# Optimization experiments

Measured on AMD Instinct MI355X. Metric: run time of the kernel, lower is better.

Reference implementation:

```python
import math
import jax, jax.numpy as jnp
import numpy as np

C = 32        # per-head dim
N_HEAD = 8
C_IN = 128

def setup_inputs() -> dict:
    key = jax.random.key(0)
    ks = jax.random.split(key, 10)
    B, S = 1, 256
    sc = 0.05  # keep logits in a sane range
    x    = jax.random.normal(ks[0], (B, S, S, C_IN), dtype=jnp.float32)
    bias = jax.random.normal(ks[1], (B, N_HEAD, S, S), dtype=jnp.float32)
    attention_mask = jax.random.randint(ks[2], (B, S, S), 0, 2).astype(bool)
    Wq = jax.random.normal(ks[3], (C_IN, C * N_HEAD), dtype=jnp.float32) * sc
    Wk = jax.random.normal(ks[4], (C_IN, C * N_HEAD), dtype=jnp.float32) * sc
    Wv = jax.random.normal(ks[5], (C_IN, C * N_HEAD), dtype=jnp.float32) * sc
    Wo = jax.random.normal(ks[6], (C * N_HEAD, C_IN), dtype=jnp.float32) * sc
    bo = jnp.zeros((C_IN,), dtype=jnp.float32)
    Wg = jax.random.normal(ks[7], (C_IN, C * N_HEAD), dtype=jnp.float32) * sc
    bg = jnp.zeros((C * N_HEAD,), dtype=jnp.float32)
    return {"x": x, "bias": bias, "attention_mask": attention_mask,
            "Wq": Wq, "Wk": Wk, "Wv": Wv, "Wo": Wo, "bo": bo, "Wg": Wg, "bg": bg}

def reference(x, bias, attention_mask, Wq, Wk, Wv, Wo, bo, Wg, bg):
    # x: [B, S, L, c_in]; attn_dim=2 is already the second-to-last dim,
    # so the torch movedim(attn_dim, -2) is the identity here.
    B, S, L, _ = x.shape
    q = x @ Wq  # [B, S, L, H*c]
    k = x @ Wk
    v = x @ Wv
    # split heads: [B, S, L, H, c] -> [B, S, H, L, c]
    def split_heads(t):
        return t.reshape(B, S, L, N_HEAD, C).transpose(0, 1, 3, 2, 4)
    q, k, v = split_heads(q), split_heads(k), split_heads(v)
    q = q / math.sqrt(C)
    # attention logits: [B, S, H, q, k]
    a = jnp.einsum('bshqc,bshkc->bshqk', q, k)
    # bias [B, H, q, k] -> broadcast over the axial batch dim S
    a = a + bias[:, None, :, :, :]
    # mask [B, S, k] -> [B, S, 1, 1, k]; masked positions get -inf
    m = attention_mask[:, :, None, None, :]
    a = jnp.where(m, a, -jnp.inf)
    a = jax.nn.softmax(a, axis=-1)
    o = jnp.einsum('bshqk,bshkc->bshqc', a, v)
    # merge heads: [B, S, H, L, c] -> [B, S, L, H*c]
    o = o.transpose(0, 1, 3, 2, 4).reshape(B, S, L, N_HEAD * C)
    # sigmoid gate
    g = jax.nn.sigmoid(x @ Wg + bg)
    o = g * o
    return o @ Wo + bo
```

## Files before the change

### kernel.cpp

```cpp
#include <hip/hip_runtime.h>
#include <hip/hip_bf16.h>
#include <cstdint>

#define CIN 128
#define NH 8
#define CH 32
#define LDQ16 1024

typedef short bf16x8 __attribute__((ext_vector_type(8)));
typedef short bf16x4 __attribute__((ext_vector_type(4)));
typedef float f32x4 __attribute__((ext_vector_type(4)));

__device__ __forceinline__ short f2bf(float f) {
  union { float f; unsigned u; } v; v.f = f;
  unsigned r = (v.u + 0x7FFFu + ((v.u >> 16) & 1u)) >> 16;
  return (short)r;
}
__device__ __forceinline__ float bf2f(short s) {
  union { unsigned u; float f; } v; v.u = ((unsigned)(unsigned short)s) << 16;
  return v.f;
}
__device__ __forceinline__ unsigned pk2bf(float a, float b) {
  union { __hip_bfloat162 h; unsigned u; } cv;
  cv.h = __float22bfloat162_rn(make_float2(a, b));
  return cv.u;
}

__global__ __launch_bounds__(256) void prep(
    const float* __restrict__ x,
    const float* __restrict__ Wq, const float* __restrict__ Wk,
    const float* __restrict__ Wv, const float* __restrict__ Wg,
    const float* __restrict__ Wo,
    const uint4* __restrict__ mask,
    short* __restrict__ xb, short* __restrict__ WT, short* __restrict__ WoT,
    unsigned int* __restrict__ flag)
{
  __shared__ int viol;
  const int b = blockIdx.x;
  if (b < 4096) {
    int base = (b * 256 + threadIdx.x) * 8;
    float4 a = *(const float4*)(x + base);
    float4 c = *(const float4*)(x + base + 4);
    bf16x8 r;
    r[0] = f2bf(a.x); r[1] = f2bf(a.y); r[2] = f2bf(a.z); r[3] = f2bf(a.w);
    r[4] = f2bf(c.x); r[5] = f2bf(c.y); r[6] = f2bf(c.z); r[7] = f2bf(c.w);
    *(bf16x8*)(xb + base) = r;
  } else if (b < 4160) {
    const float qscale = 0.17677669529663689f;
    int bb = b - 4096;
#pragma unroll
    for (int e = 0; e < 10; ++e) {
      int o = bb * 2560 + e * 256 + threadIdx.x;
      if (o < 131072) {
        int n = o >> 7, k = o & 127;
        int seg = n >> 8, nn = n & 255;
        const float* W = (seg == 0) ? Wq : (seg == 1) ? Wk : (seg == 2) ? Wv : Wg;
        float v = W[k * 256 + nn];
        if (seg == 0) v *= qscale;
        WT[o] = f2bf(v);
      } else {
        int o2 = o - 131072;
        int n = o2 >> 8, k = o2 & 255;
        WoT[o2] = f2bf(Wo[k * 128 + n]);
      }
    }
  } else {
    if (threadIdx.x == 0) viol = 0;
    __syncthreads();
    int v = 0;
#pragma unroll
    for (int j = 0; j < 16; ++j) {
      uint4 w = mask[j * 256 + threadIdx.x];
      v |= (w.x > 1u) | (w.y > 1u) | (w.z > 1u) | (w.w > 1u);
    }
    if (v) atomicOr(&viol, 1);
    __syncthreads();
    if (threadIdx.x == 0) *flag = viol ? 0u : 1u;
  }
}

__global__ __launch_bounds__(256) void proj_qkvg(
    const short* __restrict__ xb, const short* __restrict__ WT,
    const float* __restrict__ bg, short* __restrict__ qkvg)
{
  __shared__ short Al[64 * 136];
  __shared__ short Bl[128 * 136];
  const int tid = threadIdx.x;
  const int lane = tid & 63, w = tid >> 6;
  const int g = lane >> 4, c16 = lane & 15;
  const int wr = w & 1, wc = w >> 1;
  const int n0 = blockIdx.x * 128;
  const int row0 = blockIdx.y * 64;

  {
    const short* src = xb + (size_t)row0 * 128;
#pragma unroll
    for (int ch = 0; ch < 4; ++ch) {
      int c = ch * 256 + tid;
      int r = c >> 4, kc = c & 15;
      *(bf16x8*)&Al[r * 136 + kc * 8] = *(const bf16x8*)(src + r * 128 + kc * 8);
    }
    const short* wsrc = WT + (size_t)n0 * 128;
#pragma unroll
    for (int ch = 0; ch < 8; ++ch) {
      int c = ch * 256 + tid;
      int r = c >> 4, kc = c & 15;
      *(bf16x8*)&Bl[r * 136 + kc * 8] = *(const bf16x8*)(wsrc + r * 128 + kc * 8);
    }
  }
  __syncthreads();

  f32x4 acc[2][4];
#pragma unroll
  for (int rt = 0; rt < 2; ++rt)
#pragma unroll
    for (int ct = 0; ct < 4; ++ct) acc[rt][ct] = (f32x4){0.f, 0.f, 0.f, 0.f};

#pragma unroll
  for (int kk = 0; kk < 4; ++kk) {
    bf16x8 af[2], bfr[4];
#pragma unroll
    for (int rt = 0; rt < 2; ++rt)
      af[rt] = *(const bf16x8*)&Al[(wr * 32 + rt * 16 + c16) * 136 + kk * 32 + g * 8];
#pragma unroll
    for (int ct = 0; ct < 4; ++ct)
      bfr[ct] = *(const bf16x8*)&Bl[(wc * 64 + ct * 16 + c16) * 136 + kk * 32 + g * 8];
#pragma unroll
    for (int rt = 0; rt < 2; ++rt)
#pragma unroll
      for (int ct = 0; ct < 4; ++ct)
        acc[rt][ct] = __builtin_amdgcn_mfma_f32_16x16x32_bf16(af[rt], bfr[ct], acc[rt][ct], 0, 0, 0);
  }

  const int seg3 = (n0 >= 768);
  float bgv[4];
  if (seg3) {
#pragma unroll
    for (int ct = 0; ct < 4; ++ct)
      bgv[ct] = bg[n0 - 768 + wc * 64 + ct * 16 + c16];
  }
#pragma unroll
  for (int rt = 0; rt < 2; ++rt)
#pragma unroll
    for (int ct = 0; ct < 4; ++ct) {
      int col = n0 + wc * 64 + ct * 16 + c16;
#pragma unroll
      for (int i = 0; i < 4; ++i) {
        int row = row0 + wr * 32 + rt * 16 + g * 4 + i;
        float v = acc[rt][ct][i];
        if (seg3) v = 1.f / (1.f + __expf(-(v + bgv[ct])));
        qkvg[(size_t)row * LDQ16 + col] = f2bf(v);
      }
    }
}

__global__ __launch_bounds__(256, 4) void attn(
    short* __restrict__ qkvg, const float* __restrict__ bias,
    const void* __restrict__ maskraw, const unsigned int* __restrict__ flagp)
{
  __shared__ __align__(16) short lds16[19216];
  const int tid = threadIdx.x;
  const int h = blockIdx.x;
  const int srow = blockIdx.y;
  const int lane = tid & 63, w = tid >> 6;
  const int g = lane >> 4, c16 = lane & 15;
  short* rowbase = qkvg + (size_t)srow * (256 * LDQ16);
  unsigned int* vTd = (unsigned int*)&lds16[10240];
  float* lL = (float*)&lds16[18688];

  const unsigned int fl = *flagp;
  int mv = fl ? ((const int*)maskraw)[srow * 256 + tid]
              : (int)((const unsigned char*)maskraw)[srow * 256 + tid];
  unsigned long long bb = __ballot(mv != 0);
  unsigned int* scratch = (unsigned int*)&lds16[19200];
  if (lane == 0) {
    scratch[w * 2 + 0] = (unsigned int)bb;
    scratch[w * 2 + 1] = (unsigned int)(bb >> 32);
  }

#pragma unroll
  for (int it = 0; it < 2; ++it) {
    int c = it * 256 + tid;
    int kp = c >> 2, cv = c & 3;
    const short* p0 = rowbase + (size_t)(2 * kp) * LDQ16 + 256 + h * CH + cv * 8;
    bf16x8 k0 = *(const bf16x8*)p0;
    bf16x8 k1 = *(const bf16x8*)(p0 + LDQ16);
    bf16x8 v0 = *(const bf16x8*)(p0 + 256);
    bf16x8 v1 = *(const bf16x8*)(p0 + LDQ16 + 256);
    *(bf16x8*)&lds16[(2 * kp) * 40 + cv * 8] = k0;
    *(bf16x8*)&lds16[(2 * kp + 1) * 40 + cv * 8] = k1;
#pragma unroll
    for (int j = 0; j < 8; ++j)
      vTd[(cv * 8 + j) * 132 + kp] =
          ((unsigned)(unsigned short)v0[j]) | (((unsigned)(unsigned short)v1[j]) << 16);
  }

  const int qb = w * 64;
  bf16x8 qf[4];
#pragma unroll
  for (int qt = 0; qt < 4; ++qt)
    qf[qt] = *(const bf16x8*)(rowbase + (size_t)(qb + qt * 16 + c16) * LDQ16 + h * CH + g * 8);

  __syncthreads();

  unsigned int mb[8];
#pragma unroll
  for (int j = 0; j < 8; ++j) mb[j] = scratch[j];

  const f32x4 zero4 = {0.f, 0.f, 0.f, 0.f};
  float l_[4] = {0.f, 0.f, 0.f, 0.f};
  f32x4 O[4][2];
#pragma unroll
  for (int qt = 0; qt < 4; ++qt) { O[qt][0] = zero4; O[qt][1] = zero4; }

  const float* bh = bias + (size_t)h * 65536;

  for (int ch = 0; ch < 8; ++ch) {
    float4 bb4[2][4];
#pragma unroll
    for (int kt = 0; kt < 2; ++kt)
#pragma unroll
      for (int qt = 0; qt < 4; ++qt)
        bb4[kt][qt] = *(const float4*)(bh + (size_t)(qb + qt * 16 + c16) * 256 +
                                       ch * 32 + kt * 16 + g * 4);

#pragma unroll
    for (int kt = 0; kt < 2; ++kt) {
      bf16x8 kf = *(const bf16x8*)&lds16[(ch * 32 + kt * 16 + c16) * 40 + g * 8];
      bf16x4 vlo, vhi;
      {
        union { unsigned u[2]; bf16x4 v; } t0, t1;
        const unsigned* plo = &vTd[(size_t)c16 * 132 + ch * 16 + kt * 8 + g * 2];
        const unsigned* phi = &vTd[(size_t)(16 + c16) * 132 + ch * 16 + kt * 8 + g * 2];
        t0.u[0] = plo[0]; t0.u[1] = plo[1];
        t1.u[0] = phi[0]; t1.u[1] = phi[1];
        vlo = t0.v; vhi = t1.v;
      }
      const unsigned nib = (mb[ch] >> (kt * 16 + g * 4)) & 0xFu;
      float em[4];
#pragma unroll
      for (int i = 0; i < 4; ++i) em[i] = ((nib >> i) & 1u) ? 1.f : 0.f;
#pragma unroll
      for (int qt = 0; qt < 4; ++qt) {
        f32x4 S = __builtin_amdgcn_mfma_f32_16x16x32_bf16(kf, qf[qt], zero4, 0, 0, 0);
        float p0 = em[0] * __expf(fminf(S[0] + bb4[kt][qt].x, 85.f));
        float p1 = em[1] * __expf(fminf(S[1] + bb4[kt][qt].y, 85.f));
        float p2 = em[2] * __expf(fminf(S[2] + bb4[kt][qt].z, 85.f));
        float p3 = em[3] * __expf(fminf(S[3] + bb4[kt][qt].w, 85.f));
        l_[qt] += (p0 + p1) + (p2 + p3);
        union { unsigned u[2]; bf16x4 v; } pu;
        pu.u[0] = pk2bf(p0, p1);
        pu.u[1] = pk2bf(p2, p3);
        O[qt][0] = __builtin_amdgcn_mfma_f32_16x16x16bf16_1k(pu.v, vlo, O[qt][0], 0, 0, 0);
        O[qt][1] = __builtin_amdgcn_mfma_f32_16x16x16bf16_1k(pu.v, vhi, O[qt][1], 0, 0, 0);
      }
    }
  }

#pragma unroll
  for (int qt = 0; qt < 4; ++qt) {
    float v = l_[qt];
    v += __shfl_xor(v, 16);
    v += __shfl_xor(v, 32);
    if (lane < 16) lL[w * 64 + qt * 16 + c16] = v;
  }

#pragma unroll
  for (int qt = 0; qt < 4; ++qt)
#pragma unroll
    for (int i = 0; i < 4; ++i) {
      float l = lL[w * 64 + qt * 16 + g * 4 + i];
      float inv = 1.f / l;
      short* orow = rowbase + (size_t)(qb + qt * 16 + g * 4 + i) * LDQ16;
#pragma unroll
      for (int half = 0; half < 2; ++half) {
        int c = half * 16 + c16;
        float gv = bf2f(orow[768 + h * CH + c]);
        orow[h * CH + c] = f2bf(O[qt][half][i] * inv * gv);
      }
    }
}

__global__ __launch_bounds__(256) void out_proj(
    const short* __restrict__ og, const short* __restrict__ WoT,
    const float* __restrict__ bo, float* __restrict__ out)
{
  __shared__ short Al[64 * 136];
  __shared__ short Bl[128 * 136];
  const int tid = threadIdx.x;
  const int lane = tid & 63, w = tid >> 6;
  const int g = lane >> 4, c16 = lane & 15;
  const int wr = w & 1, wc = w >> 1;
  const int row0 = blockIdx.x * 64;

  f32x4 acc[2][4];
#pragma unroll
  for (int rt = 0; rt < 2; ++rt)
#pragma unroll
    for (int ct = 0; ct < 4; ++ct) acc[rt][ct] = (f32x4){0.f, 0.f, 0.f, 0.f};

  for (int kk0 = 0; kk0 < 256; kk0 += 128) {
#pragma unroll
    for (int ch = 0; ch < 4; ++ch) {
      int c = ch * 256 + tid;
      int r = c >> 4, kc = c & 15;
      *(bf16x8*)&Al[r * 136 + kc * 8] =
          *(const bf16x8*)(og + (size_t)(row0 + r) * LDQ16 + kk0 + kc * 8);
    }
#pragma unroll
    for (int ch = 0; ch < 8; ++ch) {
      int c = ch * 256 + tid;
      int r = c >> 4, kc = c & 15;
      *(bf16x8*)&Bl[r * 136 + kc * 8] =
          *(const bf16x8*)(WoT + (size_t)r * 256 + kk0 + kc * 8);
    }
    __syncthreads();
#pragma unroll
    for (int kk = 0; kk < 4; ++kk) {
      bf16x8 af[2], bfr[4];
#pragma unroll
      for (int rt = 0; rt < 2; ++rt)
        af[rt] = *(const bf16x8*)&Al[(wr * 32 + rt * 16 + c16) * 136 + kk * 32 + g * 8];
#pragma unroll
      for (int ct = 0; ct < 4; ++ct)
        bfr[ct] = *(const bf16x8*)&Bl[(wc * 64 + ct * 16 + c16) * 136 + kk * 32 + g * 8];
#pragma unroll
      for (int rt = 0; rt < 2; ++rt)
#pragma unroll
        for (int ct = 0; ct < 4; ++ct)
          acc[rt][ct] = __builtin_amdgcn_mfma_f32_16x16x32_bf16(af[rt], bfr[ct], acc[rt][ct], 0, 0, 0);
    }
    __syncthreads();
  }

#pragma unroll
  for (int rt = 0; rt < 2; ++rt)
#pragma unroll
    for (int ct = 0; ct < 4; ++ct) {
      int col = wc * 64 + ct * 16 + c16;
      float bv = bo[col];
#pragma unroll
      for (int i = 0; i < 4; ++i) {
        int row = row0 + wr * 32 + rt * 16 + g * 4 + i;
        out[(size_t)row * CIN + col] = acc[rt][ct][i] + bv;
      }
    }
}

extern "C" void kernel_launch(void* const* d_in, const int* in_sizes, int n_in,
                              void* d_out, int out_size, void* d_ws, size_t ws_size,
                              hipStream_t stream) {
  const float* x    = (const float*)d_in[0];
  const float* bias = (const float*)d_in[1];
  const void*  mask = d_in[2];
  const float* Wq   = (const float*)d_in[3];
  const float* Wk   = (const float*)d_in[4];
  const float* Wv   = (const float*)d_in[5];
  const float* Wo   = (const float*)d_in[6];
  const float* bo   = (const float*)d_in[7];
  const float* Wg   = (const float*)d_in[8];
  const float* bg   = (const float*)d_in[9];
  float* out = (float*)d_out;

  unsigned int* flag = (unsigned int*)d_ws;
  short* WT   = (short*)((char*)d_ws + 256);
  short* WoT  = WT + 131072;
  short* xb   = WoT + 32768;
  short* qkvg = xb + (size_t)65536 * 128;

  prep<<<4161, 256, 0, stream>>>(x, Wq, Wk, Wv, Wg, Wo, (const uint4*)mask,
                                 xb, WT, WoT, flag);
  proj_qkvg<<<dim3(8, 1024), 256, 0, stream>>>(xb, WT, bg, qkvg);
  attn<<<dim3(NH, 256), 256, 0, stream>>>(qkvg, bias, mask, flag);
  out_proj<<<1024, 256, 0, stream>>>(qkvg, WoT, bo, out);
}
```

Baseline: 259.8 us.

## Read K directly from global, shrink LDS, use exp2 with pre-scaled Q and bias

The attention kernel stops staging K in LDS and loads K fragments straight from global memory (L2-cached), which cuts LDS use roughly in half and lets launch bounds request 8 blocks per CU instead of 4. The softmax exponential switches from expf to exp2. To keep results unchanged, log2(e) is folded into the Q weight scale and into a pre-scaled copy of the bias produced by extra blocks in the prep kernel. In exchange, K loads now sit on the global-memory path inside the inner loop, prep does an extra pass over the bias tensor, and the higher occupancy target may squeeze registers.

```diff
diff --git a/kernel.cpp b/kernel.cpp
--- a/kernel.cpp
+++ b/kernel.cpp
@@ -30,10 +30,10 @@
     const float* __restrict__ x,
     const float* __restrict__ Wq, const float* __restrict__ Wk,
     const float* __restrict__ Wv, const float* __restrict__ Wg,
-    const float* __restrict__ Wo,
+    const float* __restrict__ Wo, const float* __restrict__ bias,
     const uint4* __restrict__ mask,
     short* __restrict__ xb, short* __restrict__ WT, short* __restrict__ WoT,
-    unsigned int* __restrict__ flag)
+    float* __restrict__ biasX, unsigned int* __restrict__ flag)
 {
   __shared__ int viol;
   const int b = blockIdx.x;
@@ -46,7 +46,7 @@
     r[4] = f2bf(c.x); r[5] = f2bf(c.y); r[6] = f2bf(c.z); r[7] = f2bf(c.w);
     *(bf16x8*)(xb + base) = r;
   } else if (b < 4160) {
-    const float qscale = 0.17677669529663689f;
+    const float qscale = 0.25504430213978686f;
     int bb = b - 4096;
 #pragma unroll
     for (int e = 0; e < 10; ++e) {
@@ -64,6 +64,12 @@
         WoT[o2] = f2bf(Wo[k * 128 + n]);
       }
     }
+  } else if (b < 4672) {
+    const float LOG2E = 1.4426950408889634f;
+    int idx = ((b - 4160) * 256 + threadIdx.x) * 4;
+    float4 v = *(const float4*)(bias + idx);
+    v.x *= LOG2E; v.y *= LOG2E; v.z *= LOG2E; v.w *= LOG2E;
+    *(float4*)(biasX + idx) = v;
   } else {
     if (threadIdx.x == 0) viol = 0;
     __syncthreads();
@@ -154,25 +160,25 @@
     }
 }
 
-__global__ __launch_bounds__(256, 4) void attn(
+__global__ __launch_bounds__(256, 8) void attn(
     short* __restrict__ qkvg, const float* __restrict__ bias,
     const void* __restrict__ maskraw, const unsigned int* __restrict__ flagp)
 {
-  __shared__ __align__(16) short lds16[19216];
+  __shared__ __align__(16) short lds16[8976];
   const int tid = threadIdx.x;
   const int h = blockIdx.x;
   const int srow = blockIdx.y;
   const int lane = tid & 63, w = tid >> 6;
   const int g = lane >> 4, c16 = lane & 15;
   short* rowbase = qkvg + (size_t)srow * (256 * LDQ16);
-  unsigned int* vTd = (unsigned int*)&lds16[10240];
-  float* lL = (float*)&lds16[18688];
+  unsigned int* vTd = (unsigned int*)&lds16[0];
+  float* lL = (float*)&lds16[8448];
+  unsigned int* scratch = (unsigned int*)&lds16[8960];
 
   const unsigned int fl = *flagp;
   int mv = fl ? ((const int*)maskraw)[srow * 256 + tid]
               : (int)((const unsigned char*)maskraw)[srow * 256 + tid];
   unsigned long long bb = __ballot(mv != 0);
-  unsigned int* scratch = (unsigned int*)&lds16[19200];
   if (lane == 0) {
     scratch[w * 2 + 0] = (unsigned int)bb;
     scratch[w * 2 + 1] = (unsigned int)(bb >> 32);
@@ -182,13 +188,9 @@
   for (int it = 0; it < 2; ++it) {
     int c = it * 256 + tid;
     int kp = c >> 2, cv = c & 3;
-    const short* p0 = rowbase + (size_t)(2 * kp) * LDQ16 + 256 + h * CH + cv * 8;
-    bf16x8 k0 = *(const bf16x8*)p0;
-    bf16x8 k1 = *(const bf16x8*)(p0 + LDQ16);
-    bf16x8 v0 = *(const bf16x8*)(p0 + 256);
-    bf16x8 v1 = *(const bf16x8*)(p0 + LDQ16 + 256);
-    *(bf16x8*)&lds16[(2 * kp) * 40 + cv * 8] = k0;
-    *(bf16x8*)&lds16[(2 * kp + 1) * 40 + cv * 8] = k1;
+    const short* p0 = rowbase + (size_t)(2 * kp) * LDQ16 + 512 + h * CH + cv * 8;
+    bf16x8 v0 = *(const bf16x8*)p0;
+    bf16x8 v1 = *(const bf16x8*)(p0 + LDQ16);
 #pragma unroll
     for (int j = 0; j < 8; ++j)
       vTd[(cv * 8 + j) * 132 + kp] =
@@ -201,6 +203,8 @@
   for (int qt = 0; qt < 4; ++qt)
     qf[qt] = *(const bf16x8*)(rowbase + (size_t)(qb + qt * 16 + c16) * LDQ16 + h * CH + g * 8);
 
+  const short* kb = rowbase + (size_t)c16 * LDQ16 + 256 + h * CH + g * 8;
+
   __syncthreads();
 
   unsigned int mb[8];
@@ -226,7 +230,7 @@
 
 #pragma unroll
     for (int kt = 0; kt < 2; ++kt) {
-      bf16x8 kf = *(const bf16x8*)&lds16[(ch * 32 + kt * 16 + c16) * 40 + g * 8];
+      bf16x8 kf = *(const bf16x8*)(kb + (size_t)((ch * 32 + kt * 16) * LDQ16));
       bf16x4 vlo, vhi;
       {
         union { unsigned u[2]; bf16x4 v; } t0, t1;
@@ -243,10 +247,10 @@
 #pragma unroll
       for (int qt = 0; qt < 4; ++qt) {
         f32x4 S = __builtin_amdgcn_mfma_f32_16x16x32_bf16(kf, qf[qt], zero4, 0, 0, 0);
-        float p0 = em[0] * __expf(fminf(S[0] + bb4[kt][qt].x, 85.f));
-        float p1 = em[1] * __expf(fminf(S[1] + bb4[kt][qt].y, 85.f));
-        float p2 = em[2] * __expf(fminf(S[2] + bb4[kt][qt].z, 85.f));
-        float p3 = em[3] * __expf(fminf(S[3] + bb4[kt][qt].w, 85.f));
+        float p0 = em[0] * __builtin_exp2f(fminf(S[0] + bb4[kt][qt].x, 122.f));
+        float p1 = em[1] * __builtin_exp2f(fminf(S[1] + bb4[kt][qt].y, 122.f));
+        float p2 = em[2] * __builtin_exp2f(fminf(S[2] + bb4[kt][qt].z, 122.f));
+        float p3 = em[3] * __builtin_exp2f(fminf(S[3] + bb4[kt][qt].w, 122.f));
         l_[qt] += (p0 + p1) + (p2 + p3);
         union { unsigned u[2]; bf16x4 v; } pu;
         pu.u[0] = pk2bf(p0, p1);
@@ -367,10 +371,11 @@
   short* WoT  = WT + 131072;
   short* xb   = WoT + 32768;
   short* qkvg = xb + (size_t)65536 * 128;
-
-  prep<<<4161, 256, 0, stream>>>(x, Wq, Wk, Wv, Wg, Wo, (const uint4*)mask,
-                                 xb, WT, WoT, flag);
+  float* biasX = (float*)(qkvg + (size_t)65536 * 1024);
+
+  prep<<<4673, 256, 0, stream>>>(x, Wq, Wk, Wv, Wg, Wo, bias, (const uint4*)mask,
+                                 xb, WT, WoT, biasX, flag);
   proj_qkvg<<<dim3(8, 1024), 256, 0, stream>>>(xb, WT, bg, qkvg);
-  attn<<<dim3(NH, 256), 256, 0, stream>>>(qkvg, bias, mask, flag);
+  attn<<<dim3(NH, 256), 256, 0, stream>>>(qkvg, biasX, mask, flag);
   out_proj<<<1024, 256, 0, stream>>>(qkvg, WoT, bo, out);
 }
```

After: 759.0 us. +192.2%, slower.

## Fuse x conversion, QKVG projection and attention into one per-row kernel

Applied to the files above, without the earlier changes.

Drops the separate x-to-bf16 pass and the QKVG projection kernel. A new fused kernel, one block of 512 threads per axial row, loads x once into LDS and computes Q, K, V and gate for each head on the fly. It then runs attention from LDS and writes only the gated output (256 columns instead of 1024). This removes the large qkvg intermediate round trip through HBM. In exchange only 256 blocks run, each with heavy LDS use, and every block re-reads the weights from global memory with heads processed serially, so occupancy and parallelism drop.

```diff
diff --git a/kernel.cpp b/kernel.cpp
--- a/kernel.cpp
+++ b/kernel.cpp
@@ -5,7 +5,6 @@
 #define CIN 128
 #define NH 8
 #define CH 32
-#define LDQ16 1024
 
 typedef short bf16x8 __attribute__((ext_vector_type(8)));
 typedef short bf16x4 __attribute__((ext_vector_type(4)));
@@ -27,30 +26,20 @@
 }
 
 __global__ __launch_bounds__(256) void prep(
-    const float* __restrict__ x,
     const float* __restrict__ Wq, const float* __restrict__ Wk,
     const float* __restrict__ Wv, const float* __restrict__ Wg,
     const float* __restrict__ Wo,
     const uint4* __restrict__ mask,
-    short* __restrict__ xb, short* __restrict__ WT, short* __restrict__ WoT,
+    short* __restrict__ WT, short* __restrict__ WoT,
     unsigned int* __restrict__ flag)
 {
   __shared__ int viol;
   const int b = blockIdx.x;
-  if (b < 4096) {
-    int base = (b * 256 + threadIdx.x) * 8;
-    float4 a = *(const float4*)(x + base);
-    float4 c = *(const float4*)(x + base + 4);
-    bf16x8 r;
-    r[0] = f2bf(a.x); r[1] = f2bf(a.y); r[2] = f2bf(a.z); r[3] = f2bf(a.w);
-    r[4] = f2bf(c.x); r[5] = f2bf(c.y); r[6] = f2bf(c.z); r[7] = f2bf(c.w);
-    *(bf16x8*)(xb + base) = r;
-  } else if (b < 4160) {
+  if (b < 64) {
     const float qscale = 0.17677669529663689f;
-    int bb = b - 4096;
 #pragma unroll
     for (int e = 0; e < 10; ++e) {
-      int o = bb * 2560 + e * 256 + threadIdx.x;
+      int o = b * 2560 + e * 256 + threadIdx.x;
       if (o < 131072) {
         int n = o >> 7, k = o & 127;
         int seg = n >> 8, nn = n & 255;
@@ -79,206 +68,266 @@
   }
 }
 
-__global__ __launch_bounds__(256) void proj_qkvg(
-    const short* __restrict__ xb, const short* __restrict__ WT,
-    const float* __restrict__ bg, short* __restrict__ qkvg)
+__global__ __launch_bounds__(512) void fused_attn(
+    const float* __restrict__ x, const short* __restrict__ WT,
+    const float* __restrict__ bias, const float* __restrict__ bg,
+    const void* __restrict__ maskraw, const unsigned int* __restrict__ flagp,
+    short* __restrict__ og)
 {
-  __shared__ short Al[64 * 136];
-  __shared__ short Bl[128 * 136];
+  __shared__ __align__(16) short xl[256 * 136];
+  __shared__ __align__(16) short kL[256 * 40];
+  __shared__ __align__(16) short vL[32 * 264];
+  __shared__ __align__(16) short qL[256 * 40];
+  __shared__ __align__(16) short gL[256 * 40];
+  __shared__ float lL[256];
+  __shared__ unsigned int scratch[8];
+
   const int tid = threadIdx.x;
+  const int srow = blockIdx.x;
   const int lane = tid & 63, w = tid >> 6;
   const int g = lane >> 4, c16 = lane & 15;
-  const int wr = w & 1, wc = w >> 1;
-  const int n0 = blockIdx.x * 128;
-  const int row0 = blockIdx.y * 64;
+  const int myrow = w * 32;
+
+  const unsigned int fl = *flagp;
+  if (tid < 256) {
+    int mv = fl ? ((const int*)maskraw)[srow * 256 + tid]
+                : (int)((const unsigned char*)maskraw)[srow * 256 + tid];
+    unsigned long long bb = __ballot(mv != 0);
+    if (lane == 0) {
+      scratch[w * 2 + 0] = (unsigned int)bb;
+      scratch[w * 2 + 1] = (unsigned int)(bb >> 32);
+    }
+  }
 
   {
-    const short* src = xb + (size_t)row0 * 128;
-#pragma unroll
-    for (int ch = 0; ch < 4; ++ch) {
-      int c = ch * 256 + tid;
-      int r = c >> 4, kc = c & 15;
-      *(bf16x8*)&Al[r * 136 + kc * 8] = *(const bf16x8*)(src + r * 128 + kc * 8);
-    }
-    const short* wsrc = WT + (size_t)n0 * 128;
-#pragma unroll
-    for (int ch = 0; ch < 8; ++ch) {
-      int c = ch * 256 + tid;
-      int r = c >> 4, kc = c & 15;
-      *(bf16x8*)&Bl[r * 136 + kc * 8] = *(const bf16x8*)(wsrc + r * 128 + kc * 8);
+    const float* xs = x + (size_t)srow * 256 * 128;
+#pragma unroll
+    for (int it = 0; it < 16; ++it) {
+      int idx = it * 512 + tid;
+      int row = idx >> 5, c4 = idx & 31;
+      float4 a = *(const float4*)(xs + (size_t)idx * 4);
+      union { unsigned u[2]; bf16x4 v; } pu;
+      pu.u[0] = pk2bf(a.x, a.y);
+      pu.u[1] = pk2bf(a.z, a.w);
+      *(bf16x4*)&xl[row * 136 + c4 * 4] = pu.v;
     }
   }
   __syncthreads();
 
-  f32x4 acc[2][4];
-#pragma unroll
-  for (int rt = 0; rt < 2; ++rt)
-#pragma unroll
-    for (int ct = 0; ct < 4; ++ct) acc[rt][ct] = (f32x4){0.f, 0.f, 0.f, 0.f};
-
-#pragma unroll
-  for (int kk = 0; kk < 4; ++kk) {
-    bf16x8 af[2], bfr[4];
-#pragma unroll
-    for (int rt = 0; rt < 2; ++rt)
-      af[rt] = *(const bf16x8*)&Al[(wr * 32 + rt * 16 + c16) * 136 + kk * 32 + g * 8];
-#pragma unroll
-    for (int ct = 0; ct < 4; ++ct)
-      bfr[ct] = *(const bf16x8*)&Bl[(wc * 64 + ct * 16 + c16) * 136 + kk * 32 + g * 8];
-#pragma unroll
-    for (int rt = 0; rt < 2; ++rt)
-#pragma unroll
-      for (int ct = 0; ct < 4; ++ct)
-        acc[rt][ct] = __builtin_amdgcn_mfma_f32_16x16x32_bf16(af[rt], bfr[ct], acc[rt][ct], 0, 0, 0);
+  unsigned int mb[8];
+#pragma unroll
+  for (int j = 0; j < 8; ++j) mb[j] = scratch[j];
+
+  const f32x4 zero4 = {0.f, 0.f, 0.f, 0.f};
+
+#pragma unroll 1
+  for (int h = 0; h < 8; ++h) {
+    {
+      f32x4 acc[2][2];
+#pragma unroll
+      for (int ct = 0; ct < 2; ++ct)
+#pragma unroll
+        for (int rt = 0; rt < 2; ++rt) acc[ct][rt] = zero4;
+#pragma unroll
+      for (int kk = 0; kk < 4; ++kk) {
+        bf16x8 wf[2], xf[2];
+#pragma unroll
+        for (int ct = 0; ct < 2; ++ct)
+          wf[ct] = *(const bf16x8*)(WT + (size_t)(256 + h * CH + ct * 16 + c16) * 128 + kk * 32 + g * 8);
+#pragma unroll
+        for (int rt = 0; rt < 2; ++rt)
+          xf[rt] = *(const bf16x8*)&xl[(myrow + rt * 16 + c16) * 136 + kk * 32 + g * 8];
+#pragma unroll
+        for (int ct = 0; ct < 2; ++ct)
+#pragma unroll
+          for (int rt = 0; rt < 2; ++rt)
+            acc[ct][rt] = __builtin_amdgcn_mfma_f32_16x16x32_bf16(wf[ct], xf[rt], acc[ct][rt], 0, 0, 0);
+      }
+#pragma unroll
+      for (int ct = 0; ct < 2; ++ct)
+#pragma unroll
+        for (int rt = 0; rt < 2; ++rt) {
+          union { unsigned u[2]; bf16x4 v; } pu;
+          pu.u[0] = pk2bf(acc[ct][rt][0], acc[ct][rt][1]);
+          pu.u[1] = pk2bf(acc[ct][rt][2], acc[ct][rt][3]);
+          *(bf16x4*)&kL[(myrow + rt * 16 + c16) * 40 + ct * 16 + g * 4] = pu.v;
+        }
+    }
+    {
+      f32x4 acc[2][2];
+#pragma unroll
+      for (int rt = 0; rt < 2; ++rt)
+#pragma unroll
+        for (int ct = 0; ct < 2; ++ct) acc[rt][ct] = zero4;
+#pragma unroll
+      for (int kk = 0; kk < 4; ++kk) {
+        bf16x8 wf[2], xf[2];
+#pragma unroll
+        for (int ct = 0; ct < 2; ++ct)
+          wf[ct] = *(const bf16x8*)(WT + (size_t)(512 + h * CH + ct * 16 + c16) * 128 + kk * 32 + g * 8);
+#pragma unroll
+        for (int rt = 0; rt < 2; ++rt)
+          xf[rt] = *(const bf16x8*)&xl[(myrow + rt * 16 + c16) * 136 + kk * 32 + g * 8];
+#pragma unroll
+        for (int rt = 0; rt < 2; ++rt)
+#pragma unroll
+          for (int ct = 0; ct < 2; ++ct)
+            acc[rt][ct] = __builtin_amdgcn_mfma_f32_16x16x32_bf16(xf[rt], wf[ct], acc[rt][ct], 0, 0, 0);
+      }
+#pragma unroll
+      for (int rt = 0; rt < 2; ++rt)
+#pragma unroll
+        for (int ct = 0; ct < 2; ++ct) {
+          union { unsigned u[2]; bf16x4 v; } pu;
+          pu.u[0] = pk2bf(acc[rt][ct][0], acc[rt][ct][1]);
+          pu.u[1] = pk2bf(acc[rt][ct][2], acc[rt][ct][3]);
+          *(bf16x4*)&vL[(ct * 16 + c16) * 264 + myrow + rt * 16 + g * 4] = pu.v;
+        }
+    }
+    {
+      f32x4 acc[2][2];
+#pragma unroll
+      for (int ct = 0; ct < 2; ++ct)
+#pragma unroll
+        for (int rt = 0; rt < 2; ++rt) acc[ct][rt] = zero4;
+#pragma unroll
+      for (int kk = 0; kk < 4; ++kk) {
+        bf16x8 wf[2], xf[2];
+#pragma unroll
+        for (int ct = 0; ct < 2; ++ct)
+          wf[ct] = *(const bf16x8*)(WT + (size_t)(0 + h * CH + ct * 16 + c16) * 128 + kk * 32 + g * 8);
+#pragma unroll
+        for (int rt = 0; rt < 2; ++rt)
+          xf[rt] = *(const bf16x8*)&xl[(myrow + rt * 16 + c16) * 136 + kk * 32 + g * 8];
+#pragma unroll
+        for (int ct = 0; ct < 2; ++ct)
+#pragma unroll
+          for (int rt = 0; rt < 2; ++rt)
+            acc[ct][rt] = __builtin_amdgcn_mfma_f32_16x16x32_bf16(wf[ct], xf[rt], acc[ct][rt], 0, 0, 0);
+      }
+#pragma unroll
+      for (int ct = 0; ct < 2; ++ct)
+#pragma unroll
+        for (int rt = 0; rt < 2; ++rt) {
+          union { unsigned u[2]; bf16x4 v; } pu;
+          pu.u[0] = pk2bf(acc[ct][rt][0], acc[ct][rt][1]);
+          pu.u[1] = pk2bf(acc[ct][rt][2], acc[ct][rt][3]);
+          *(bf16x4*)&qL[(myrow + rt * 16 + c16) * 40 + ct * 16 + g * 4] = pu.v;
+        }
+    }
+    {
+      f32x4 acc[2][2];
+#pragma unroll
+      for (int ct = 0; ct < 2; ++ct)
+#pragma unroll
+        for (int rt = 0; rt < 2; ++rt) acc[ct][rt] = zero4;
+#pragma unroll
+      for (int kk = 0; kk < 4; ++kk) {
+        bf16x8 wf[2], xf[2];
+#pragma unroll
+        for (int ct = 0; ct < 2; ++ct)
+          wf[ct] = *(const bf16x8*)(WT + (size_t)(768 + h * CH + ct * 16 + c16) * 128 + kk * 32 + g * 8);
+#pragma unroll
+        for (int rt = 0; rt < 2; ++rt)
+          xf[rt] = *(const bf16x8*)&xl[(myrow + rt * 16 + c16) * 136 + kk * 32 + g * 8];
+#pragma unroll
+        for (int ct = 0; ct < 2; ++ct)
+#pragma unroll
+          for (int rt = 0; rt < 2; ++rt)
+            acc[ct][rt] = __builtin_amdgcn_mfma_f32_16x16x32_bf16(wf[ct], xf[rt], acc[ct][rt], 0, 0, 0);
+      }
+#pragma unroll
+      for (int ct = 0; ct < 2; ++ct) {
+        float4 bgv = *(const float4*)(bg + h * CH + ct * 16 + g * 4);
+#pragma unroll
+        for (int rt = 0; rt < 2; ++rt) {
+          float v0 = 1.f / (1.f + __expf(-(acc[ct][rt][0] + bgv.x)));
+          float v1 = 1.f / (1.f + __expf(-(acc[ct][rt][1] + bgv.y)));
+          float v2 = 1.f / (1.f + __expf(-(acc[ct][rt][2] + bgv.z)));
+          float v3 = 1.f / (1.f + __expf(-(acc[ct][rt][3] + bgv.w)));
+          union { unsigned u[2]; bf16x4 v; } pu;
+          pu.u[0] = pk2bf(v0, v1);
+          pu.u[1] = pk2bf(v2, v3);
+          *(bf16x4*)&gL[(myrow + rt * 16 + c16) * 40 + ct * 16 + g * 4] = pu.v;
+        }
+      }
+    }
+    __syncthreads();
+
+    const int qb = myrow;
+    bf16x8 qf[2];
+#pragma unroll
+    for (int qt = 0; qt < 2; ++qt)
+      qf[qt] = *(const bf16x8*)&qL[(qb + qt * 16 + c16) * 40 + g * 8];
+
+    float l_[2] = {0.f, 0.f};
+    f32x4 O[2][2];
+#pragma unroll
+    for (int qt = 0; qt < 2; ++qt) { O[qt][0] = zero4; O[qt][1] = zero4; }
+
+    const float* bh = bias + (size_t)h * 65536;
+
+#pragma unroll 1
+    for (int ch = 0; ch < 8; ++ch) {
+      float4 bb4[2][2];
+#pragma unroll
+      for (int kt = 0; kt < 2; ++kt)
+#pragma unroll
+        for (int qt = 0; qt < 2; ++qt)
+          bb4[kt][qt] = *(const float4*)(bh + (size_t)(qb + qt * 16 + c16) * 256 +
+                                         ch * 32 + kt * 16 + g * 4);
+
+#pragma unroll
+      for (int kt = 0; kt < 2; ++kt) {
+        bf16x8 kf = *(const bf16x8*)&kL[(ch * 32 + kt * 16 + c16) * 40 + g * 8];
+        bf16x4 vlo = *(const bf16x4*)&vL[(size_t)c16 * 264 + ch * 32 + kt * 16 + g * 4];
+        bf16x4 vhi = *(const bf16x4*)&vL[(size_t)(16 + c16) * 264 + ch * 32 + kt * 16 + g * 4];
+        const unsigned nib = (mb[ch] >> (kt * 16 + g * 4)) & 0xFu;
+        float em[4];
+#pragma unroll
+        for (int i = 0; i < 4; ++i) em[i] = ((nib >> i) & 1u) ? 1.f : 0.f;
+#pragma unroll
+        for (int qt = 0; qt < 2; ++qt) {
+          f32x4 S = __builtin_amdgcn_mfma_f32_16x16x32_bf16(kf, qf[qt], zero4, 0, 0, 0);
+          float p0 = em[0] * __expf(fminf(S[0] + bb4[kt][qt].x, 85.f));
+          float p1 = em[1] * __expf(fminf(S[1] + bb4[kt][qt].y, 85.f));
+          float p2 = em[2] * __expf(fminf(S[2] + bb4[kt][qt].z, 85.f));
+          float p3 = em[3] * __expf(fminf(S[3] + bb4[kt][qt].w, 85.f));
+          l_[qt] += (p0 + p1) + (p2 + p3);
+          union { unsigned u[2]; bf16x4 v; } pu;
+          pu.u[0] = pk2bf(p0, p1);
+          pu.u[1] = pk2bf(p2, p3);
+          O[qt][0] = __builtin_amdgcn_mfma_f32_16x16x16bf16_1k(pu.v, vlo, O[qt][0], 0, 0, 0);
+          O[qt][1] = __builtin_amdgcn_mfma_f32_16x16x16bf16_1k(pu.v, vhi, O[qt][1], 0, 0, 0);
+        }
+      }
+    }
+
+#pragma unroll
+    for (int qt = 0; qt < 2; ++qt) {
+      float v = l_[qt];
+      v += __shfl_xor(v, 16);
+      v += __shfl_xor(v, 32);
+      if (lane < 16) lL[myrow + qt * 16 + c16] = v;
+    }
+
+#pragma unroll
+    for (int qt = 0; qt < 2; ++qt)
+#pragma unroll
+      for (int i = 0; i < 4; ++i) {
+        float l = lL[myrow + qt * 16 + g * 4 + i];
+        float inv = 1.f / l;
+        int row = qb + qt * 16 + g * 4 + i;
+        short* orow = og + ((size_t)srow * 256 + row) * 256 + h * CH;
+#pragma unroll
+        for (int half = 0; half < 2; ++half) {
+          int c = half * 16 + c16;
+          float gv = bf2f(gL[row * 40 + c]);
+          orow[c] = f2bf(O[qt][half][i] * inv * gv);
+        }
+      }
+    __syncthreads();
   }
-
-  const int seg3 = (n0 >= 768);
-  float bgv[4];
-  if (seg3) {
-#pragma unroll
-    for (int ct = 0; ct < 4; ++ct)
-      bgv[ct] = bg[n0 - 768 + wc * 64 + ct * 16 + c16];
-  }
-#pragma unroll
-  for (int rt = 0; rt < 2; ++rt)
-#pragma unroll
-    for (int ct = 0; ct < 4; ++ct) {
-      int col = n0 + wc * 64 + ct * 16 + c16;
-#pragma unroll
-      for (int i = 0; i < 4; ++i) {
-        int row = row0 + wr * 32 + rt * 16 + g * 4 + i;
-        float v = acc[rt][ct][i];
-        if (seg3) v = 1.f / (1.f + __expf(-(v + bgv[ct])));
-        qkvg[(size_t)row * LDQ16 + col] = f2bf(v);
-      }
-    }
-}
-
-__global__ __launch_bounds__(256, 4) void attn(
-    short* __restrict__ qkvg, const float* __restrict__ bias,
-    const void* __restrict__ maskraw, const unsigned int* __restrict__ flagp)
-{
-  __shared__ __align__(16) short lds16[19216];
-  const int tid = threadIdx.x;
-  const int h = blockIdx.x;
-  const int srow = blockIdx.y;
-  const int lane = tid & 63, w = tid >> 6;
-  const int g = lane >> 4, c16 = lane & 15;
-  short* rowbase = qkvg + (size_t)srow * (256 * LDQ16);
-  unsigned int* vTd = (unsigned int*)&lds16[10240];
-  float* lL = (float*)&lds16[18688];
-
-  const unsigned int fl = *flagp;
-  int mv = fl ? ((const int*)maskraw)[srow * 256 + tid]
-              : (int)((const unsigned char*)maskraw)[srow * 256 + tid];
-  unsigned long long bb = __ballot(mv != 0);
-  unsigned int* scratch = (unsigned int*)&lds16[19200];
-  if (lane == 0) {
-    scratch[w * 2 + 0] = (unsigned int)bb;
-    scratch[w * 2 + 1] = (unsigned int)(bb >> 32);
-  }
-
-#pragma unroll
-  for (int it = 0; it < 2; ++it) {
-    int c = it * 256 + tid;
-    int kp = c >> 2, cv = c & 3;
-    const short* p0 = rowbase + (size_t)(2 * kp) * LDQ16 + 256 + h * CH + cv * 8;
-    bf16x8 k0 = *(const bf16x8*)p0;
-    bf16x8 k1 = *(const bf16x8*)(p0 + LDQ16);
-    bf16x8 v0 = *(const bf16x8*)(p0 + 256);
-    bf16x8 v1 = *(const bf16x8*)(p0 + LDQ16 + 256);
-    *(bf16x8*)&lds16[(2 * kp) * 40 + cv * 8] = k0;
-    *(bf16x8*)&lds16[(2 * kp + 1) * 40 + cv * 8] = k1;
-#pragma unroll
-    for (int j = 0; j < 8; ++j)
-      vTd[(cv * 8 + j) * 132 + kp] =
-          ((unsigned)(unsigned short)v0[j]) | (((unsigned)(unsigned short)v1[j]) << 16);
-  }
-
-  const int qb = w * 64;
-  bf16x8 qf[4];
-#pragma unroll
-  for (int qt = 0; qt < 4; ++qt)
-    qf[qt] = *(const bf16x8*)(rowbase + (size_t)(qb + qt * 16 + c16) * LDQ16 + h * CH + g * 8);
-
-  __syncthreads();
-
-  unsigned int mb[8];
-#pragma unroll
-  for (int j = 0; j < 8; ++j) mb[j] = scratch[j];
-
-  const f32x4 zero4 = {0.f, 0.f, 0.f, 0.f};
-  float l_[4] = {0.f, 0.f, 0.f, 0.f};
-  f32x4 O[4][2];
-#pragma unroll
-  for (int qt = 0; qt < 4; ++qt) { O[qt][0] = zero4; O[qt][1] = zero4; }
-
-  const float* bh = bias + (size_t)h * 65536;
-
-  for (int ch = 0; ch < 8; ++ch) {
-    float4 bb4[2][4];
-#pragma unroll
-    for (int kt = 0; kt < 2; ++kt)
-#pragma unroll
-      for (int qt = 0; qt < 4; ++qt)
-        bb4[kt][qt] = *(const float4*)(bh + (size_t)(qb + qt * 16 + c16) * 256 +
-                                       ch * 32 + kt * 16 + g * 4);
-
-#pragma unroll
-    for (int kt = 0; kt < 2; ++kt) {
-      bf16x8 kf = *(const bf16x8*)&lds16[(ch * 32 + kt * 16 + c16) * 40 + g * 8];
-      bf16x4 vlo, vhi;
-      {
-        union { unsigned u[2]; bf16x4 v; } t0, t1;
-        const unsigned* plo = &vTd[(size_t)c16 * 132 + ch * 16 + kt * 8 + g * 2];
-        const unsigned* phi = &vTd[(size_t)(16 + c16) * 132 + ch * 16 + kt * 8 + g * 2];
-        t0.u[0] = plo[0]; t0.u[1] = plo[1];
-        t1.u[0] = phi[0]; t1.u[1] = phi[1];
-        vlo = t0.v; vhi = t1.v;
-      }
-      const unsigned nib = (mb[ch] >> (kt * 16 + g * 4)) & 0xFu;
-      float em[4];
-#pragma unroll
-      for (int i = 0; i < 4; ++i) em[i] = ((nib >> i) & 1u) ? 1.f : 0.f;
-#pragma unroll
-      for (int qt = 0; qt < 4; ++qt) {
-        f32x4 S = __builtin_amdgcn_mfma_f32_16x16x32_bf16(kf, qf[qt], zero4, 0, 0, 0);
-        float p0 = em[0] * __expf(fminf(S[0] + bb4[kt][qt].x, 85.f));
-        float p1 = em[1] * __expf(fminf(S[1] + bb4[kt][qt].y, 85.f));
-        float p2 = em[2] * __expf(fminf(S[2] + bb4[kt][qt].z, 85.f));
-        float p3 = em[3] * __expf(fminf(S[3] + bb4[kt][qt].w, 85.f));
-        l_[qt] += (p0 + p1) + (p2 + p3);
-        union { unsigned u[2]; bf16x4 v; } pu;
-        pu.u[0] = pk2bf(p0, p1);
-        pu.u[1] = pk2bf(p2, p3);
-        O[qt][0] = __builtin_amdgcn_mfma_f32_16x16x16bf16_1k(pu.v, vlo, O[qt][0], 0, 0, 0);
-        O[qt][1] = __builtin_amdgcn_mfma_f32_16x16x16bf16_1k(pu.v, vhi, O[qt][1], 0, 0, 0);
-      }
-    }
-  }
-
-#pragma unroll
-  for (int qt = 0; qt < 4; ++qt) {
-    float v = l_[qt];
-    v += __shfl_xor(v, 16);
-    v += __shfl_xor(v, 32);
-    if (lane < 16) lL[w * 64 + qt * 16 + c16] = v;
-  }
-
-#pragma unroll
-  for (int qt = 0; qt < 4; ++qt)
-#pragma unroll
-    for (int i = 0; i < 4; ++i) {
-      float l = lL[w * 64 + qt * 16 + g * 4 + i];
-      float inv = 1.f / l;
-      short* orow = rowbase + (size_t)(qb + qt * 16 + g * 4 + i) * LDQ16;
-#pragma unroll
-      for (int half = 0; half < 2; ++half) {
-        int c = half * 16 + c16;
-        float gv = bf2f(orow[768 + h * CH + c]);
-        orow[h * CH + c] = f2bf(O[qt][half][i] * inv * gv);
-      }
-    }
 }
 
 __global__ __launch_bounds__(256) void out_proj(
@@ -305,7 +354,7 @@
       int c = ch * 256 + tid;
       int r = c >> 4, kc = c & 15;
       *(bf16x8*)&Al[r * 136 + kc * 8] =
-          *(const bf16x8*)(og + (size_t)(row0 + r) * LDQ16 + kk0 + kc * 8);
+          *(const bf16x8*)(og + (size_t)(row0 + r) * 256 + kk0 + kc * 8);
     }
 #pragma unroll
     for (int ch = 0; ch < 8; ++ch) {
@@ -363,14 +412,12 @@
   float* out = (float*)d_out;
 
   unsigned int* flag = (unsigned int*)d_ws;
-  short* WT   = (short*)((char*)d_ws + 256);
-  short* WoT  = WT + 131072;
-  short* xb   = WoT + 32768;
-  short* qkvg = xb + (size_t)65536 * 128;
-
-  prep<<<4161, 256, 0, stream>>>(x, Wq, Wk, Wv, Wg, Wo, (const uint4*)mask,
-                                 xb, WT, WoT, flag);
-  proj_qkvg<<<dim3(8, 1024), 256, 0, stream>>>(xb, WT, bg, qkvg);
-  attn<<<dim3(NH, 256), 256, 0, stream>>>(qkvg, bias, mask, flag);
-  out_proj<<<1024, 256, 0, stream>>>(qkvg, WoT, bo, out);
-}
+  short* WT  = (short*)((char*)d_ws + 256);
+  short* WoT = WT + 131072;
+  short* og  = WoT + 32768;
+
+  prep<<<65, 256, 0, stream>>>(Wq, Wk, Wv, Wg, Wo, (const uint4*)mask,
+                               WT, WoT, flag);
+  fused_attn<<<256, 512, 0, stream>>>(x, WT, bias, bg, mask, flag, og);
+  out_proj<<<1024, 256, 0, stream>>>(og, WoT, bo, out);
+}
```

After: 245.7 us. -5.4%, faster.
